# Optimization experiments

Measured on AMD Instinct MI355X. Metric: run time of the kernel, lower is better.

The kernel has to match this reference:

```python
import jax, jax.numpy as jnp
import numpy as np

N_USERS = 100000
M_ITEMS = 200000
N_NODES = N_USERS + M_ITEMS
N_EDGES = 1200000
D = 64
N_LAYERS = 3
BATCH = 4096


def setup_inputs() -> dict:
    key = jax.random.key(0)
    ks = jax.random.split(key, 11)
    return {
        "users": jax.random.randint(ks[0], (BATCH,), 0, N_USERS),
        "items": jax.random.randint(ks[1], (BATCH,), 0, M_ITEMS),
        "rows": jax.random.randint(ks[2], (N_EDGES,), 0, N_NODES),
        "cols": jax.random.randint(ks[3], (N_EDGES,), 0, N_NODES),
        "vals": jax.random.uniform(ks[4], (N_EDGES,), dtype=jnp.float32),
        "user_emb": jax.random.normal(ks[5], (N_USERS, D), dtype=jnp.float32) * 0.1,
        "item_emb": jax.random.normal(ks[6], (M_ITEMS, D), dtype=jnp.float32) * 0.1,
        "W_gc": jax.random.normal(ks[7], (N_LAYERS, D, D), dtype=jnp.float32) * 0.1,
        "b_gc": jax.random.normal(ks[8], (N_LAYERS, D), dtype=jnp.float32) * 0.1,
        "W_bi": jax.random.normal(ks[9], (N_LAYERS, D, D), dtype=jnp.float32) * 0.1,
        "b_bi": jax.random.normal(ks[10], (N_LAYERS, D), dtype=jnp.float32) * 0.1,
    }


def _spmm(rows, cols, vals, x):
    # sparse.mm(Graph, x): out[r] = sum_e vals[e] * x[cols[e]] for rows[e]==r
    gathered = vals[:, None] * x[cols]  # [E, D]
    return jax.ops.segment_sum(gathered, rows, num_segments=N_NODES)


def _computer(rows, cols, vals, user_emb, item_emb, W_gc, b_gc, W_bi, b_bi):
    ego = jnp.concatenate([user_emb, item_emb], axis=0)  # [N, D]
    embs = [ego]
    for k in range(N_LAYERS):
        side = _spmm(rows, cols, vals, ego)
        sum_emb = side @ W_gc[k] + b_gc[k]
        bi_emb = (ego * side) @ W_bi[k] + b_bi[k]
        ego = jax.nn.leaky_relu(sum_emb + bi_emb, negative_slope=0.2)
        nrm = jnp.linalg.norm(ego, axis=1, keepdims=True)
        ego = ego / jnp.maximum(nrm, 1e-12)
        embs.append(ego)
    mean_emb = jnp.mean(jnp.stack(embs, axis=1), axis=1)  # [N, D]
    return mean_emb[:N_USERS], mean_emb[N_USERS:]


def reference(users, items, rows, cols, vals, user_emb, item_emb, W_gc, b_gc, W_bi, b_bi):
    all_users, all_items = _computer(rows, cols, vals, user_emb, item_emb, W_gc, b_gc, W_bi, b_bi)
    u = all_users[users]  # [B, D]
    i = all_items[items]  # [B, D]
    return jnp.sum(u * i, axis=1)  # [B]
```

## Files before the change

### kernel.cpp

```cpp
#include <hip/hip_runtime.h>
#include <hip/hip_bf16.h>

#define N_USERS 100000
#define M_ITEMS 200000
#define N_NODES 300000
#define N_EDGES 1200000
#define BATCH   4096
#define NB      ((N_NODES + 255) / 256)
#define CHUNK   5
#define EPT4    (N_EDGES / 4)
#define EGRID4  ((EPT4 + 255) / 256)

typedef __attribute__((ext_vector_type(8))) short short8;
typedef __attribute__((ext_vector_type(4))) float floatx4;

static __device__ __forceinline__ float b2f(__hip_bfloat16 x) { return __bfloat162float(x); }

static __device__ __forceinline__ short f2bs(float f) {
    union { __hip_bfloat16 h; short s; } u;
    u.h = __float2bfloat16(f);
    return u.s;
}
static __device__ __forceinline__ float us2f(unsigned int us) {
    return __uint_as_float(us << 16);
}

static __device__ __forceinline__ float loadf(const void* p, int i, int isbf) {
    if (isbf) return b2f(((const __hip_bfloat16*)p)[i]);
    return ((const float*)p)[i];
}

static __device__ __forceinline__ int sniff_dev(const void* vals) {
    const unsigned short* v16 = (const unsigned short*)vals;
    int c = 0;
#pragma unroll
    for (int i = 0; i < 16; ++i) {
        unsigned int ub = (v16[2 * i] >> 8) & 0xFF;
        if (ub >= 0x3A && ub <= 0x3F) ++c;
    }
    return (c >= 12) ? 1 : 0;
}

static __device__ __forceinline__ void unpack8(float* o, uint4 e) {
    unsigned int w[4] = {e.x, e.y, e.z, e.w};
#pragma unroll
    for (int j = 0; j < 8; ++j) o[j] = us2f((w[j >> 1] >> ((j & 1) * 16)) & 0xFFFFu);
}

static __device__ __forceinline__ const unsigned short* bfsrc(
    const void* ue, const void* ie, int n64) {
    return (n64 < N_USERS * 64)
        ? (const unsigned short*)ue + (size_t)(unsigned)n64
        : (const unsigned short*)ie + (size_t)(unsigned)(n64 - N_USERS * 64);
}
static __device__ __forceinline__ const float* fsrc(
    const void* ue, const void* ie, int n64) {
    return (n64 < N_USERS * 64)
        ? (const float*)ue + (size_t)(unsigned)n64
        : (const float*)ie + (size_t)(unsigned)(n64 - N_USERS * 64);
}

static __device__ __forceinline__ void gather16o(
    float* o0, float* o1, const unsigned short* ego,
    const void* ue, const void* ie, int n64, int quad, int isbf, int use_src) {
    if (!use_src) {
        const unsigned short* p = ego + (size_t)(unsigned)n64 + quad * 8;
        unpack8(o0, *(const uint4*)p);
        unpack8(o1, *(const uint4*)(p + 32));
    } else if (isbf) {
        const unsigned short* p = bfsrc(ue, ie, n64) + quad * 8;
        unpack8(o0, *(const uint4*)p);
        unpack8(o1, *(const uint4*)(p + 32));
    } else {
        const float* p = fsrc(ue, ie, n64) + quad * 8;
        float4 a = *(const float4*)p;
        float4 b = *(const float4*)(p + 4);
        float4 c = *(const float4*)(p + 32);
        float4 d = *(const float4*)(p + 36);
        o0[0]=a.x; o0[1]=a.y; o0[2]=a.z; o0[3]=a.w; o0[4]=b.x; o0[5]=b.y; o0[6]=b.z; o0[7]=b.w;
        o1[0]=c.x; o1[1]=c.y; o1[2]=c.z; o1[3]=c.w; o1[4]=d.x; o1[5]=d.y; o1[6]=d.z; o1[7]=d.w;
    }
}

__global__ __launch_bounds__(256) void setup_kernel(
    const void* __restrict__ Wg, const void* __restrict__ bg,
    const void* __restrict__ Wb, const void* __restrict__ bb,
    const void* __restrict__ vals,
    const int* __restrict__ users, const int* __restrict__ items,
    unsigned short* __restrict__ WT, float* __restrict__ sb,
    unsigned char* __restrict__ f1, unsigned char* __restrict__ f2,
    unsigned char* __restrict__ f3) {
    if (blockIdx.x < 12) {
        int isbf = __builtin_amdgcn_readfirstlane(sniff_dev(vals));
        int t = blockIdx.x * 256 + threadIdx.x;
        if (t < 3072) {
            int lane = t & 63, h = (t >> 6) & 1, ct = (t >> 7) & 3, w = (t >> 9) & 1, k = t >> 10;
            int m = lane & 15, quad = lane >> 4;
            const void* Wsrc = w ? Wb : Wg;
#pragma unroll
            for (int j = 0; j < 8; ++j) {
                int kk = h * 32 + quad * 8 + j;
                WT[(size_t)(k * 1024 + w * 512 + ct * 128 + h * 64 + lane) * 8 + j] =
                    (unsigned short)f2bs(loadf(Wsrc, k * 4096 + kk * 64 + ct * 16 + m, isbf));
            }
        }
        if (t < 192) sb[t] = loadf(bg, t, isbf) + loadf(bb, t, isbf);
    } else {
        int i = (blockIdx.x - 12) * 256 + threadIdx.x;
        int n = -1;
        if (i < BATCH) n = users[i];
        else if (i < 2 * BATCH) n = N_USERS + items[i - BATCH];
        if (n >= 0) { f1[n] = 1; f2[n] = 1; f3[n] = 1; }
    }
}

__global__ __launch_bounds__(256) void prop_kernel(
    const int4* __restrict__ rows4, const int4* __restrict__ cols4,
    const unsigned char* __restrict__ src, unsigned char* __restrict__ dst) {
    int t = blockIdx.x * 256 + threadIdx.x;
    if (t < EPT4) {
        int4 r = rows4[t];
        int4 c = cols4[t];
        if (src[r.x]) dst[c.x] = 1;
        if (src[r.y]) dst[c.y] = 1;
        if (src[r.z]) dst[c.z] = 1;
        if (src[r.w]) dst[c.w] = 1;
    }
}

__global__ __launch_bounds__(256) void count_rank_kernel(
    const int4* __restrict__ rows4, const unsigned char* __restrict__ flag1,
    int* __restrict__ off, uint2* __restrict__ rank) {
    int t = blockIdx.x * 256 + threadIdx.x;
    if (t < EPT4) {
        int4 r = rows4[t];
        unsigned int k0 = 0xFFFFu, k1 = 0xFFFFu, k2 = 0xFFFFu, k3 = 0xFFFFu;
        if (flag1[r.x]) k0 = (unsigned int)atomicAdd(&off[r.x + 1], 1);
        if (flag1[r.y]) k1 = (unsigned int)atomicAdd(&off[r.y + 1], 1);
        if (flag1[r.z]) k2 = (unsigned int)atomicAdd(&off[r.z + 1], 1);
        if (flag1[r.w]) k3 = (unsigned int)atomicAdd(&off[r.w + 1], 1);
        rank[t] = make_uint2((k0 & 0xFFFFu) | (k1 << 16), (k2 & 0xFFFFu) | (k3 << 16));
    }
}

static __device__ __forceinline__ int deg_class(int d) {
    return d >= 16 ? 0 : d >= 8 ? 1 : d >= 4 ? 2 : 3;
}

__global__ __launch_bounds__(256) void scanA_kernel(
    const int* __restrict__ off, const unsigned char* __restrict__ flags,
    int* __restrict__ bsum, int* __restrict__ bcnt, unsigned char* __restrict__ cls) {
    __shared__ int s[256];
    __shared__ int w[4];
    int t = threadIdx.x;
    int n = blockIdx.x * 256 + t;
    bool ir = (n < N_NODES);
    int deg = ir ? off[n + 1] : 0;
    s[t] = deg;
    __syncthreads();
    for (int o = 128; o >= 1; o >>= 1) {
        if (t < o) s[t] += s[t + o];
        __syncthreads();
    }
    if (t == 0) bsum[blockIdx.x] = s[0];
    int c = deg_class(deg);
    if (ir) cls[n] = (unsigned char)c;
    int lane = t & 63;
    int wid  = t >> 6;
#pragma unroll
    for (int L = 0; L < 3; ++L) {
        bool fl = ir && flags[L * N_NODES + n];
#pragma unroll
        for (int cc = 0; cc < 4; ++cc) {
            unsigned long long mask = __ballot(fl && (c == cc));
            if (lane == 0) w[wid] = __popcll(mask);
            __syncthreads();
            if (t == 0) bcnt[(L * 4 + cc) * NB + blockIdx.x] = w[0] + w[1] + w[2] + w[3];
            __syncthreads();
        }
    }
}

__global__ __launch_bounds__(256) void scanB13_kernel(
    int* __restrict__ bsum, int* __restrict__ bcnt, int* __restrict__ vtot) {
    __shared__ int s[256];
    int t = threadIdx.x;
    int* A = (blockIdx.x < 12) ? (bcnt + (size_t)blockIdx.x * NB) : bsum;
    int base = t * CHUNK, loc = 0;
    for (int j = 0; j < CHUNK; ++j) { int i = base + j; if (i < NB) loc += A[i]; }
    s[t] = loc;
    __syncthreads();
    for (int o = 1; o < 256; o <<= 1) {
        int add = (t >= o) ? s[t - o] : 0;
        __syncthreads();
        s[t] += add;
        __syncthreads();
    }
    int run = (t == 0) ? 0 : s[t - 1];
    for (int j = 0; j < CHUNK; ++j) {
        int i = base + j;
        if (i < NB) { int tmp = A[i]; A[i] = run; run += tmp; }
    }
    if (blockIdx.x < 12 && t == 0) vtot[blockIdx.x] = s[255];
}

__global__ __launch_bounds__(256) void scanC_kernel(
    int* __restrict__ off, const int* __restrict__ bsum,
    const unsigned char* __restrict__ flags, const unsigned char* __restrict__ cls,
    const int* __restrict__ bcnt, const int* __restrict__ vtot,
    int* __restrict__ lists, int* __restrict__ map3, int* __restrict__ cnts) {
    __shared__ int s[256];
    __shared__ int wsum[4];
    __shared__ int vb[12];
    int t = threadIdx.x;
    if (t < 12) {
        int L = t >> 2, c = t & 3;
        int b = 0;
        for (int cc = 0; cc < c; ++cc) b += vtot[L * 4 + cc];
        vb[t] = b;
    }
    if (blockIdx.x == 0 && t < 3)
        cnts[t] = vtot[t * 4] + vtot[t * 4 + 1] + vtot[t * 4 + 2] + vtot[t * 4 + 3];
    int n = blockIdx.x * 256 + t;
    bool ir = (n < N_NODES);
    s[t] = ir ? off[n + 1] : 0;
    __syncthreads();
    for (int o = 1; o < 256; o <<= 1) {
        int add = (t >= o) ? s[t - o] : 0;
        __syncthreads();
        s[t] += add;
        __syncthreads();
    }
    if (ir) off[n + 1] = s[t] + bsum[blockIdx.x];
    int c = ir ? (int)cls[n] : 3;
    int lane = t & 63;
    int wid  = t >> 6;
#pragma unroll
    for (int L = 0; L < 3; ++L) {
        bool fl = ir && flags[L * N_NODES + n];
#pragma unroll
        for (int cc = 0; cc < 4; ++cc) {
            bool f = fl && (c == cc);
            unsigned long long mask = __ballot(f);
            if (lane == 0) wsum[wid] = __popcll(mask);
            __syncthreads();
            int base = bcnt[(L * 4 + cc) * NB + blockIdx.x] + vb[L * 4 + cc];
            for (int i = 0; i < wid; ++i) base += wsum[i];
            if (f) {
                int pos = base + __popcll(mask & ((1ull << lane) - 1ull));
                lists[L * N_NODES + pos] = n;
                if (L == 2) map3[n] = pos + 1;
            }
            __syncthreads();
        }
    }
}

__global__ __launch_bounds__(256) void fill_kernel(
    const int4* __restrict__ rows4, const int4* __restrict__ cols4,
    const void* __restrict__ vals, const int* __restrict__ off,
    const uint2* __restrict__ rank, int2* __restrict__ epack) {
    int isbf = __builtin_amdgcn_readfirstlane(sniff_dev(vals));
    int t = blockIdx.x * 256 + threadIdx.x;
    if (t < EPT4) {
        int4 r = rows4[t];
        int4 c = cols4[t];
        uint2 kk = rank[t];
        unsigned int k0 = kk.x & 0xFFFFu, k1 = kk.x >> 16;
        unsigned int k2 = kk.y & 0xFFFFu, k3 = kk.y >> 16;
        int e = t * 4;
        if (k0 != 0xFFFFu)
            epack[off[r.x] + (int)k0] = make_int2(c.x << 6, __float_as_int(loadf(vals, e, isbf)));
        if (k1 != 0xFFFFu)
            epack[off[r.y] + (int)k1] = make_int2(c.y << 6, __float_as_int(loadf(vals, e + 1, isbf)));
        if (k2 != 0xFFFFu)
            epack[off[r.z] + (int)k2] = make_int2(c.z << 6, __float_as_int(loadf(vals, e + 2, isbf)));
        if (k3 != 0xFFFFu)
            epack[off[r.w] + (int)k3] = make_int2(c.w << 6, __float_as_int(loadf(vals, e + 3, isbf)));
    }
}

template<int USE_SRC>
__global__ __launch_bounds__(256) void fused_layer_kernel(
    const int* __restrict__ off, const int2* __restrict__ epack,
    const unsigned short* __restrict__ ego_in,
    const void* __restrict__ ue, const void* __restrict__ ie,
    const void* __restrict__ vals,
    const unsigned short* __restrict__ WT, const float* __restrict__ sb,
    int klayer, unsigned short* __restrict__ ego_out,
    const int* __restrict__ list, const int* __restrict__ cntp,
    const int* __restrict__ map3, float* __restrict__ acc) {
    const int isbf = USE_SRC ? __builtin_amdgcn_readfirstlane(sniff_dev(vals)) : 0;
    const int cnt  = __builtin_amdgcn_readfirstlane(cntp[0]);
    const int ntile = (cnt + 15) >> 4;
    const int lane = threadIdx.x & 63;
    const int m    = lane & 15;
    const int quad = lane >> 4;

    const unsigned short* wt = WT + (size_t)klayer * 8192;
    short8 Bg[4][2], Bb[4][2];
#pragma unroll
    for (int ct = 0; ct < 4; ++ct)
#pragma unroll
        for (int h = 0; h < 2; ++h) {
            Bg[ct][h] = *(const short8*)(wt + (size_t)((ct * 2 + h) * 64 + lane) * 8);
            Bb[ct][h] = *(const short8*)(wt + (size_t)(512 + (ct * 2 + h) * 64 + lane) * 8);
        }
    float bv[4];
#pragma unroll
    for (int ct = 0; ct < 4; ++ct) bv[ct] = sb[klayer * 64 + ct * 16 + m];

    const int wv = blockIdx.x * 4 + (threadIdx.x >> 6);
    const int nw = gridDim.x * 4;
    for (int tile = wv; tile < ntile; tile += nw) {
        const int idx = tile * 16 + m;
        const int row = list[idx < cnt ? idx : cnt - 1];
        const int start = off[row];
        const int end   = off[row + 1];

        float eg0[8], eg1[8];
        gather16o(eg0, eg1, ego_in, ue, ie, row << 6, quad, isbf, USE_SRC);

        float s0[8] = {0,0,0,0,0,0,0,0};
        float s1[8] = {0,0,0,0,0,0,0,0};
        for (int e = start; e < end; ++e) {
            int2 cv = epack[e];
            float v = __int_as_float(cv.y);
            float t0[8], t1[8];
            gather16o(t0, t1, ego_in, ue, ie, cv.x, quad, isbf, USE_SRC);
#pragma unroll
            for (int j = 0; j < 8; ++j) {
                s0[j] = fmaf(v, t0[j], s0[j]);
                s1[j] = fmaf(v, t1[j], s1[j]);
            }
        }

        short8 As0, As1, Ap0, Ap1;
#pragma unroll
        for (int j = 0; j < 8; ++j) {
            As0[j] = f2bs(s0[j]);
            As1[j] = f2bs(s1[j]);
            Ap0[j] = f2bs(eg0[j] * s0[j]);
            Ap1[j] = f2bs(eg1[j] * s1[j]);
        }

        floatx4 accf[4];
#pragma unroll
        for (int ct = 0; ct < 4; ++ct) {
            floatx4 a = {0.f, 0.f, 0.f, 0.f};
            a = __builtin_amdgcn_mfma_f32_16x16x32_bf16(As0, Bg[ct][0], a, 0, 0, 0);
            a = __builtin_amdgcn_mfma_f32_16x16x32_bf16(As1, Bg[ct][1], a, 0, 0, 0);
            a = __builtin_amdgcn_mfma_f32_16x16x32_bf16(Ap0, Bb[ct][0], a, 0, 0, 0);
            a = __builtin_amdgcn_mfma_f32_16x16x32_bf16(Ap1, Bb[ct][1], a, 0, 0, 0);
            accf[ct] = a;
        }

        float v[4][4];
        float ssq[4] = {0.f, 0.f, 0.f, 0.f};
#pragma unroll
        for (int ct = 0; ct < 4; ++ct)
#pragma unroll
            for (int r = 0; r < 4; ++r) {
                float x = accf[ct][r] + bv[ct];
                x = x > 0.f ? x : 0.2f * x;
                v[ct][r] = x;
                ssq[r] += x * x;
            }
#pragma unroll
        for (int o = 1; o < 16; o <<= 1)
#pragma unroll
            for (int r = 0; r < 4; ++r) ssq[r] += __shfl_xor(ssq[r], o, 64);
#pragma unroll
        for (int r = 0; r < 4; ++r) {
            int idx_w = tile * 16 + quad * 4 + r;
            if (idx_w < cnt) {
                float sc = 1.0f / fmaxf(sqrtf(ssq[r]), 1e-12f);
                int rw = list[idx_w];
                int c3 = map3[rw];
#pragma unroll
                for (int ct = 0; ct < 4; ++ct)
                    ego_out[(size_t)rw * 64 + ct * 16 + m] = (unsigned short)f2bs(v[ct][r] * sc);
                if (c3 > 0) {
                    float* ap = acc + (size_t)(c3 - 1) * 64 + m;
#pragma unroll
                    for (int ct = 0; ct < 4; ++ct) ap[ct * 16] += v[ct][r] * sc;
                }
            }
        }
    }
}

__global__ __launch_bounds__(256) void dot_kernel(
    const int* __restrict__ users, const int* __restrict__ items,
    const float* __restrict__ acc, const int* __restrict__ map3,
    const void* __restrict__ ue, const void* __restrict__ ie,
    void* __restrict__ out, const void* __restrict__ vals) {
    int isbf = __builtin_amdgcn_readfirstlane(sniff_dev(vals));
    int gid = blockIdx.x * 256 + threadIdx.x;
    int b = gid >> 6;
    int lane = gid & 63;
    int un = __builtin_amdgcn_readfirstlane(users[b]);
    int in_ = __builtin_amdgcn_readfirstlane(items[b]);
    int cu = __builtin_amdgcn_readfirstlane(map3[un]);
    int ci = __builtin_amdgcn_readfirstlane(map3[N_USERS + in_]);
    float u = (cu > 0 ? acc[(size_t)(cu - 1) * 64 + lane] : 0.f) + loadf(ue, un * 64 + lane, isbf);
    float v = (ci > 0 ? acc[(size_t)(ci - 1) * 64 + lane] : 0.f) + loadf(ie, in_ * 64 + lane, isbf);
    float pr = u * v;
#pragma unroll
    for (int o = 32; o >= 1; o >>= 1) pr += __shfl_xor(pr, o, 64);
    if (lane == 0) {
        float r = pr * 0.0625f;
        if (isbf) ((__hip_bfloat16*)out)[b] = __float2bfloat16(r);
        else      ((float*)out)[b] = r;
    }
}

static inline size_t align16(size_t x) { return (x + 15) & ~(size_t)15; }

extern "C" void kernel_launch(void* const* d_in, const int* in_sizes, int n_in,
                              void* d_out, int out_size, void* d_ws, size_t ws_size,
                              hipStream_t stream) {
    const int* users = (const int*)d_in[0];
    const int* items = (const int*)d_in[1];
    const int* rows  = (const int*)d_in[2];
    const int* cols  = (const int*)d_in[3];
    const void* vals     = d_in[4];
    const void* user_emb = d_in[5];
    const void* item_emb = d_in[6];
    const void* W_gc     = d_in[7];
    const void* b_gc     = d_in[8];
    const void* W_bi     = d_in[9];
    const void* b_bi     = d_in[10];

    const size_t egoB   = (size_t)N_NODES * 64 * sizeof(short);
    const size_t packB  = (size_t)N_EDGES * sizeof(int2);
    const size_t rankB  = (size_t)EPT4 * sizeof(uint2);
    const size_t bsumB  = (size_t)NB * sizeof(int);
    const size_t bcntB  = (size_t)12 * NB * sizeof(int);
    const size_t clsB   = (size_t)N_NODES;
    const size_t wtB    = (size_t)3 * 1024 * 8 * sizeof(short);
    const size_t sbB    = (size_t)192 * sizeof(float);
    const size_t accB   = (size_t)2 * BATCH * 64 * sizeof(float);
    const size_t offB   = (size_t)(N_NODES + 1) * sizeof(int);
    const size_t cntsB  = (size_t)32 * sizeof(int);
    const size_t map3B  = (size_t)N_NODES * sizeof(int);
    const size_t flagsB = (size_t)3 * N_NODES;

    char* ws = (char*)d_ws;
    size_t o = 0;
    unsigned short* egoA  = (unsigned short*)(ws + o); o += egoB;
    unsigned short* egoB2 = (unsigned short*)(ws + o); o += egoB;
    int2*  epack  = (int2*)(ws + o);  o += packB;
    uint2* rank   = (uint2*)(ws + o); o += rankB;
    int*   bsum   = (int*)(ws + o);   o += bsumB;
    int*   bcnt   = (int*)(ws + o);   o += bcntB;
    unsigned char* cls = (unsigned char*)(ws + o); o += clsB;
    o = align16(o);
    unsigned short* WT = (unsigned short*)(ws + o); o += wtB;
    float* sb     = (float*)(ws + o); o += sbB;
    o = align16(o);
    float* acc    = (float*)(ws + o);
    int*   off    = (int*)((char*)acc + accB);
    int*   cnts   = (int*)((char*)off + offB);
    int*   vtot   = cnts + 4;
    int*   map3   = (int*)((char*)cnts + cntsB);
    unsigned char* flags = (unsigned char*)((char*)map3 + map3B);
    const size_t zeroB = accB + offB + cntsB + map3B + flagsB;
    unsigned char* flagL[3] = {flags, flags + N_NODES, flags + 2 * N_NODES};
    int* lists = (int*)(flags + flagsB);
    int* listL[3] = {lists, lists + N_NODES, lists + 2 * N_NODES};

    hipMemsetAsync(acc, 0, zeroB, stream);

    setup_kernel<<<44, 256, 0, stream>>>(W_gc, b_gc, W_bi, b_bi, vals, users, items,
                                         WT, sb, flagL[0], flagL[1], flagL[2]);

    prop_kernel<<<EGRID4, 256, 0, stream>>>((const int4*)rows, (const int4*)cols, flagL[2], flagL[1]);
    prop_kernel<<<EGRID4, 256, 0, stream>>>((const int4*)rows, (const int4*)cols, flagL[1], flagL[0]);

    count_rank_kernel<<<EGRID4, 256, 0, stream>>>((const int4*)rows, flagL[0], off, rank);

    scanA_kernel<<<NB, 256, 0, stream>>>(off, flags, bsum, bcnt, cls);
    scanB13_kernel<<<13, 256, 0, stream>>>(bsum, bcnt, vtot);
    scanC_kernel<<<NB, 256, 0, stream>>>(off, bsum, flags, cls, bcnt, vtot, lists, map3, cnts);

    fill_kernel<<<EGRID4, 256, 0, stream>>>((const int4*)rows, (const int4*)cols, vals, off, rank, epack);

    fused_layer_kernel<1><<<2048, 256, 0, stream>>>(off, epack, egoA, user_emb, item_emb,
                                                    vals, WT, sb, 0, egoA,
                                                    listL[0], cnts + 0, map3, acc);
    fused_layer_kernel<0><<<2048, 256, 0, stream>>>(off, epack, egoA, user_emb, item_emb,
                                                    vals, WT, sb, 1, egoB2,
                                                    listL[1], cnts + 1, map3, acc);
    fused_layer_kernel<0><<<2048, 256, 0, stream>>>(off, epack, egoB2, user_emb, item_emb,
                                                    vals, WT, sb, 2, egoA,
                                                    listL[2], cnts + 2, map3, acc);
    dot_kernel<<<(BATCH * 64) / 256, 256, 0, stream>>>(users, items, acc, map3,
                                                       user_emb, item_emb, d_out, vals);
}
```

Before: 280.7 us.

## Skip col loads in flag propagation, cut scan barriers, use one-wave blocks

The flag-propagation kernel now reads the four source flags first and loads the column indices only when at least one flag is set, which avoids useless col traffic. The scan kernels compute per-class ballot masks once and combine them with a single flag ballot per layer, reducing the syncthreads pairs from twelve to three. The fused layer kernel moves to 64-thread single-wave blocks with 8192 blocks and exits early when there is no tile, aiming at finer scheduling and less tail imbalance. The trade-off is more block launches and a loss of any reuse the weight preload got from sharing a larger block.

```diff
diff --git a/kernel.cpp b/kernel.cpp
--- a/kernel.cpp
+++ b/kernel.cpp
@@ -120,11 +120,14 @@
     int t = blockIdx.x * 256 + threadIdx.x;
     if (t < EPT4) {
         int4 r = rows4[t];
-        int4 c = cols4[t];
-        if (src[r.x]) dst[c.x] = 1;
-        if (src[r.y]) dst[c.y] = 1;
-        if (src[r.z]) dst[c.z] = 1;
-        if (src[r.w]) dst[c.w] = 1;
+        unsigned char s0 = src[r.x], s1 = src[r.y], s2 = src[r.z], s3 = src[r.w];
+        if (s0 | s1 | s2 | s3) {
+            int4 c = cols4[t];
+            if (s0) dst[c.x] = 1;
+            if (s1) dst[c.y] = 1;
+            if (s2) dst[c.z] = 1;
+            if (s3) dst[c.w] = 1;
+        }
     }
 }
 
@@ -151,7 +154,7 @@
     const int* __restrict__ off, const unsigned char* __restrict__ flags,
     int* __restrict__ bsum, int* __restrict__ bcnt, unsigned char* __restrict__ cls) {
     __shared__ int s[256];
-    __shared__ int w[4];
+    __shared__ int wc[4][4];
     int t = threadIdx.x;
     int n = blockIdx.x * 256 + t;
     bool ir = (n < N_NODES);
@@ -167,17 +170,20 @@
     if (ir) cls[n] = (unsigned char)c;
     int lane = t & 63;
     int wid  = t >> 6;
+    unsigned long long mc[4];
+#pragma unroll
+    for (int cc = 0; cc < 4; ++cc) mc[cc] = __ballot(ir && (c == cc));
 #pragma unroll
     for (int L = 0; L < 3; ++L) {
-        bool fl = ir && flags[L * N_NODES + n];
-#pragma unroll
-        for (int cc = 0; cc < 4; ++cc) {
-            unsigned long long mask = __ballot(fl && (c == cc));
-            if (lane == 0) w[wid] = __popcll(mask);
-            __syncthreads();
-            if (t == 0) bcnt[(L * 4 + cc) * NB + blockIdx.x] = w[0] + w[1] + w[2] + w[3];
-            __syncthreads();
-        }
+        unsigned long long mf = __ballot(ir && flags[L * N_NODES + n]);
+        if (lane == 0) {
+#pragma unroll
+            for (int cc = 0; cc < 4; ++cc) wc[wid][cc] = __popcll(mf & mc[cc]);
+        }
+        __syncthreads();
+        if (t < 4)
+            bcnt[(L * 4 + t) * NB + blockIdx.x] = wc[0][t] + wc[1][t] + wc[2][t] + wc[3][t];
+        __syncthreads();
     }
 }
 
@@ -210,7 +216,7 @@
     const int* __restrict__ bcnt, const int* __restrict__ vtot,
     int* __restrict__ lists, int* __restrict__ map3, int* __restrict__ cnts) {
     __shared__ int s[256];
-    __shared__ int wsum[4];
+    __shared__ int wc[4][4];
     __shared__ int vb[12];
     int t = threadIdx.x;
     if (t < 12) {
@@ -235,24 +241,28 @@
     int c = ir ? (int)cls[n] : 3;
     int lane = t & 63;
     int wid  = t >> 6;
+    unsigned long long mc[4];
+#pragma unroll
+    for (int cc = 0; cc < 4; ++cc) mc[cc] = __ballot(ir && (c == cc));
+    unsigned long long lt = (1ull << lane) - 1ull;
 #pragma unroll
     for (int L = 0; L < 3; ++L) {
         bool fl = ir && flags[L * N_NODES + n];
-#pragma unroll
-        for (int cc = 0; cc < 4; ++cc) {
-            bool f = fl && (c == cc);
-            unsigned long long mask = __ballot(f);
-            if (lane == 0) wsum[wid] = __popcll(mask);
-            __syncthreads();
-            int base = bcnt[(L * 4 + cc) * NB + blockIdx.x] + vb[L * 4 + cc];
-            for (int i = 0; i < wid; ++i) base += wsum[i];
-            if (f) {
-                int pos = base + __popcll(mask & ((1ull << lane) - 1ull));
-                lists[L * N_NODES + pos] = n;
-                if (L == 2) map3[n] = pos + 1;
-            }
-            __syncthreads();
-        }
+        unsigned long long mf = __ballot(fl);
+        if (lane == 0) {
+#pragma unroll
+            for (int cc = 0; cc < 4; ++cc) wc[wid][cc] = __popcll(mf & mc[cc]);
+        }
+        __syncthreads();
+        if (fl) {
+            int wpre = 0;
+            for (int i = 0; i < wid; ++i) wpre += wc[i][c];
+            int pos = bcnt[(L * 4 + c) * NB + blockIdx.x] + vb[L * 4 + c] + wpre
+                    + __popcll(mf & mc[c] & lt);
+            lists[L * N_NODES + pos] = n;
+            if (L == 2) map3[n] = pos + 1;
+        }
+        __syncthreads();
     }
 }
 
@@ -281,7 +291,7 @@
 }
 
 template<int USE_SRC>
-__global__ __launch_bounds__(256) void fused_layer_kernel(
+__global__ __launch_bounds__(64) void fused_layer_kernel(
     const int* __restrict__ off, const int2* __restrict__ epack,
     const unsigned short* __restrict__ ego_in,
     const void* __restrict__ ue, const void* __restrict__ ie,
@@ -293,7 +303,10 @@
     const int isbf = USE_SRC ? __builtin_amdgcn_readfirstlane(sniff_dev(vals)) : 0;
     const int cnt  = __builtin_amdgcn_readfirstlane(cntp[0]);
     const int ntile = (cnt + 15) >> 4;
-    const int lane = threadIdx.x & 63;
+    const int wv = blockIdx.x;
+    const int nw = gridDim.x;
+    if (wv >= ntile) return;
+    const int lane = threadIdx.x;
     const int m    = lane & 15;
     const int quad = lane >> 4;
 
@@ -310,8 +323,6 @@
 #pragma unroll
     for (int ct = 0; ct < 4; ++ct) bv[ct] = sb[klayer * 64 + ct * 16 + m];
 
-    const int wv = blockIdx.x * 4 + (threadIdx.x >> 6);
-    const int nw = gridDim.x * 4;
     for (int tile = wv; tile < ntile; tile += nw) {
         const int idx = tile * 16 + m;
         const int row = list[idx < cnt ? idx : cnt - 1];
@@ -486,15 +497,15 @@
 
     fill_kernel<<<EGRID4, 256, 0, stream>>>((const int4*)rows, (const int4*)cols, vals, off, rank, epack);
 
-    fused_layer_kernel<1><<<2048, 256, 0, stream>>>(off, epack, egoA, user_emb, item_emb,
-                                                    vals, WT, sb, 0, egoA,
-                                                    listL[0], cnts + 0, map3, acc);
-    fused_layer_kernel<0><<<2048, 256, 0, stream>>>(off, epack, egoA, user_emb, item_emb,
-                                                    vals, WT, sb, 1, egoB2,
-                                                    listL[1], cnts + 1, map3, acc);
-    fused_layer_kernel<0><<<2048, 256, 0, stream>>>(off, epack, egoB2, user_emb, item_emb,
-                                                    vals, WT, sb, 2, egoA,
-                                                    listL[2], cnts + 2, map3, acc);
+    fused_layer_kernel<1><<<8192, 64, 0, stream>>>(off, epack, egoA, user_emb, item_emb,
+                                                   vals, WT, sb, 0, egoA,
+                                                   listL[0], cnts + 0, map3, acc);
+    fused_layer_kernel<0><<<8192, 64, 0, stream>>>(off, epack, egoA, user_emb, item_emb,
+                                                   vals, WT, sb, 1, egoB2,
+                                                   listL[1], cnts + 1, map3, acc);
+    fused_layer_kernel<0><<<8192, 64, 0, stream>>>(off, epack, egoB2, user_emb, item_emb,
+                                                   vals, WT, sb, 2, egoA,
+                                                   listL[2], cnts + 2, map3, acc);
     dot_kernel<<<(BATCH * 64) / 256, 256, 0, stream>>>(users, items, acc, map3,
                                                        user_emb, item_emb, d_out, vals);
 }
```

Result: no change. 277.4 us (median of 2 runs) (-1.2%).
